# Optimization experiments

Hardware: AMD Instinct MI355X
Metric: run time of the kernel (lower is better)

The kernel has to match this reference:

```python
import jax, jax.numpy as jnp
import numpy as np

DIM = 1024

def setup_inputs() -> dict:
    key = jax.random.key(0)
    ks = jax.random.split(key, 7)
    s = 1.0 / np.sqrt(DIM)
    x = jax.random.normal(ks[0], (8, 2048, DIM), dtype=jnp.float32)
    Wq = jax.random.uniform(ks[1], (DIM, DIM), jnp.float32, -s, s)
    bq = jax.random.uniform(ks[2], (DIM,), jnp.float32, -s, s)
    Wk = jax.random.uniform(ks[3], (DIM, DIM), jnp.float32, -s, s)
    bk = jax.random.uniform(ks[4], (DIM,), jnp.float32, -s, s)
    Wv = jax.random.uniform(ks[5], (DIM, DIM), jnp.float32, -s, s)
    bv = jax.random.uniform(ks[6], (DIM,), jnp.float32, -s, s)
    return {"x": x, "Wq": Wq, "bq": bq, "Wk": Wk, "bk": bk, "Wv": Wv, "bv": bv}

def reference(x, Wq, bq, Wk, bk, Wv, bv):
    # nn.Linear: y = x @ W.T + b
    q = jnp.einsum('bsd,ed->bse', x, Wq) + bq  # [B,S,D]
    k = jnp.einsum('bsd,ed->bse', x, Wk) + bk
    v = jnp.einsum('bsd,ed->bse', x, Wv) + bv
    scores = jnp.einsum('bqd,bkd->bqk', q, k) / jnp.sqrt(jnp.float32(DIM))
    attn = jax.nn.softmax(scores, axis=-1)
    return jnp.einsum('bqk,bkd->bqd', attn, v)
```

## Files before the change

### kernel.cpp

```cpp
#include <hip/hip_runtime.h>

#define DIM 1024
#define SEQ 2048

typedef __attribute__((ext_vector_type(8))) short bf16x8;
typedef __attribute__((ext_vector_type(4))) float f32x4;
typedef __attribute__((ext_vector_type(4))) unsigned short us4;
typedef __attribute__((ext_vector_type(4))) _Float16 h4;

__device__ __forceinline__ unsigned short f2bf(float f) {
    union { float f; unsigned int u; } v; v.f = f;
    unsigned int r = (v.u + 0x7FFFu + ((v.u >> 16) & 1u)) >> 16;
    return (unsigned short)r;
}

#define GLOAD(gp, lp) __builtin_amdgcn_global_load_lds( \
    (const __attribute__((address_space(1))) unsigned int*)(gp), \
    (__attribute__((address_space(3))) unsigned int*)(lp), 16, 0, 0)

__global__ __launch_bounds__(256) void cast_f32_bf16(const float* __restrict__ src,
                                                     unsigned short* __restrict__ dst, int n) {
    int i = (blockIdx.x * 256 + threadIdx.x) * 8;
    if (i >= n) return;
    float4 a = *(const float4*)(src + i);
    float4 b = *(const float4*)(src + i + 4);
    us4 lo = { f2bf(a.x), f2bf(a.y), f2bf(a.z), f2bf(a.w) };
    us4 hi = { f2bf(b.x), f2bf(b.y), f2bf(b.z), f2bf(b.w) };
    *(us4*)(dst + i) = lo;
    *(us4*)(dst + i + 4) = hi;
}

#define STAGE4(sb, kt) do { \
    GLOAD(A + (size_t)(lr) * lda + (kt) + csrc,       smem + (sb) * 32768 + wid * 1024); \
    GLOAD(A + (size_t)(128 + lr) * lda + (kt) + csrc, smem + (sb) * 32768 + 8192 + wid * 1024); \
    GLOAD(B + (size_t)(lr) * ldb + (kt) + csrc,       smem + (sb) * 32768 + 16384 + wid * 1024); \
    GLOAD(B + (size_t)(128 + lr) * ldb + (kt) + csrc, smem + (sb) * 32768 + 24576 + wid * 1024); \
} while (0)

__device__ __forceinline__ void gemm256_core(
    const unsigned short* __restrict__ A, const unsigned short* __restrict__ B,
    int lda, int ldb, int K, char* smem, f32x4 acc[8][4])
{
    const int tid = threadIdx.x;
    const int lane = tid & 63;
    const int wid = tid >> 6;
    const int wm = wid >> 2;
    const int wn = wid & 3;
    const int lr = tid >> 2;
    const int csrc = ((tid & 3) ^ ((tid >> 3) & 3)) * 8;

    int aoff[8], boff[4];
    {
        int arow = wm * 128 + (lane & 15);
        int cr = (lane >> 4) ^ ((arow >> 1) & 3);
#pragma unroll
        for (int mi = 0; mi < 8; mi++) aoff[mi] = (arow + mi * 16) * 64 + cr * 16;
        int brow = wn * 64 + (lane & 15);
        int crb = (lane >> 4) ^ ((brow >> 1) & 3);
#pragma unroll
        for (int nj = 0; nj < 4; nj++) boff[nj] = 16384 + (brow + nj * 16) * 64 + crb * 16;
    }

    const int nph = K >> 5;

#pragma unroll
    for (int jb = 0; jb < 3; jb++) STAGE4(jb, jb * 32);

    for (int j = 0; j < nph; ++j) {
        if (j + 2 < nph)      asm volatile("s_waitcnt vmcnt(8)" ::: "memory");
        else if (j + 1 < nph) asm volatile("s_waitcnt vmcnt(4)" ::: "memory");
        else                  asm volatile("s_waitcnt vmcnt(0)" ::: "memory");
        __builtin_amdgcn_s_barrier();

        const char* bufb = smem + (j & 3) * 32768;
        bf16x8 af[8], bfr[4];
#pragma unroll
        for (int mi = 0; mi < 8; mi++) af[mi] = *(const bf16x8*)(bufb + aoff[mi]);
#pragma unroll
        for (int nj = 0; nj < 4; nj++) bfr[nj] = *(const bf16x8*)(bufb + boff[nj]);

        if (j + 3 < nph) STAGE4((j + 3) & 3, (j + 3) * 32);

        __builtin_amdgcn_s_setprio(1);
#pragma unroll
        for (int mi = 0; mi < 8; mi++)
#pragma unroll
            for (int nj = 0; nj < 4; nj++)
                acc[mi][nj] = __builtin_amdgcn_mfma_f32_16x16x32_bf16(af[mi], bfr[nj], acc[mi][nj], 0, 0, 0);
        __builtin_amdgcn_s_setprio(0);
    }
}

#define ACC_INIT() \
    f32x4 acc[8][4]; \
    _Pragma("unroll") for (int i = 0; i < 8; i++) \
    _Pragma("unroll") for (int jj = 0; jj < 4; jj++) acc[i][jj] = (f32x4){0.f, 0.f, 0.f, 0.f};

__global__ __launch_bounds__(512, 2) void gemm_qkv(
    const unsigned short* __restrict__ xb, const unsigned short* __restrict__ wb,
    const float* __restrict__ bq, const float* __restrict__ bk, const float* __restrict__ bv,
    unsigned short* __restrict__ qb, unsigned short* __restrict__ kb, unsigned short* __restrict__ vt)
{
    extern __shared__ char smem[];
    const int bid = blockIdx.x;
    const int lb = (bid & 7) * 96 + (bid >> 3);
    const int bz = lb >> 8;
    const int r = lb & 255;
    const int m0 = (r >> 2) * 256, n0 = (r & 3) * 256;
    const float* bias = (bz == 0) ? bq : ((bz == 1) ? bk : bv);
    ACC_INIT();
    gemm256_core(xb + (size_t)m0 * DIM, wb + (size_t)bz * DIM * DIM + (size_t)n0 * DIM,
                 DIM, DIM, DIM, smem, acc);
    const int lane = threadIdx.x & 63, wid = threadIdx.x >> 6;
    const int wm = wid >> 2, wn = wid & 3;
    const float scale = (bz == 0) ? 0.03125f : 1.0f;
    unsigned short* C = (bz == 0) ? qb : kb;
#pragma unroll
    for (int mig = 0; mig < 8; mig++)
#pragma unroll
        for (int nj = 0; nj < 4; nj++) {
            int col = n0 + wn * 64 + nj * 16 + (lane & 15);
            float bcol = bias[col];
#pragma unroll
            for (int rr = 0; rr < 4; rr++) {
                int row = m0 + wm * 128 + mig * 16 + (lane >> 4) * 4 + rr;
                float v = (acc[mig][nj][rr] + bcol) * scale;
                if (bz < 2) {
                    C[(size_t)row * DIM + col] = f2bf(v);
                } else {
                    int b = row >> 11, s = row & 2047;
                    vt[((size_t)b << 21) + ((size_t)col << 11) + s] = f2bf(v);
                }
            }
        }
}

__global__ __launch_bounds__(512, 2) void gemm_qk(
    const unsigned short* __restrict__ qb, const unsigned short* __restrict__ kb,
    unsigned short* __restrict__ sb)
{
    extern __shared__ char smem[];
    const int bid = blockIdx.x;
    const int lb = (bid & 7) * 64 + (bid >> 3);
    const int b = lb >> 6;
    const int r = lb & 63;
    const int m0 = (r >> 3) * 256, n0 = (r & 7) * 256;
    ACC_INIT();
    gemm256_core(qb + ((size_t)b * SEQ + m0) * DIM, kb + ((size_t)b * SEQ + n0) * DIM,
                 DIM, DIM, DIM, smem, acc);
    const int lane = threadIdx.x & 63, wid = threadIdx.x >> 6;
    const int wm = wid >> 2, wn = wid & 3;
    _Float16* sh = (_Float16*)sb + (size_t)b * SEQ * SEQ;
#pragma unroll
    for (int mig = 0; mig < 8; mig++)
#pragma unroll
        for (int nj = 0; nj < 4; nj++) {
            int col = n0 + wn * 64 + nj * 16 + (lane & 15);
#pragma unroll
            for (int rr = 0; rr < 4; rr++) {
                int row = m0 + wm * 128 + mig * 16 + (lane >> 4) * 4 + rr;
                sh[(size_t)row * SEQ + col] = (_Float16)acc[mig][nj][rr];
            }
        }
}

__global__ __launch_bounds__(256) void softmax_p(unsigned short* __restrict__ sb)
{
    const int lane = threadIdx.x & 63, wid = threadIdx.x >> 6;
    const size_t row = (size_t)blockIdx.x * 4 + wid;
    unsigned short* rp = sb + row * SEQ;
    float v[32];
#pragma unroll
    for (int j = 0; j < 8; j++) {
        h4 h = *(const h4*)(rp + (j * 64 + lane) * 4);
#pragma unroll
        for (int e = 0; e < 4; e++) v[j * 4 + e] = (float)h[e];
    }
    float m = -1e30f;
#pragma unroll
    for (int i = 0; i < 32; i++) m = fmaxf(m, v[i]);
#pragma unroll
    for (int msk = 1; msk <= 32; msk <<= 1) m = fmaxf(m, __shfl_xor(m, msk, 64));
    float s = 0.f;
#pragma unroll
    for (int i = 0; i < 32; i++) { v[i] = __expf(v[i] - m); s += v[i]; }
#pragma unroll
    for (int msk = 1; msk <= 32; msk <<= 1) s += __shfl_xor(s, msk, 64);
    float inv = 1.0f / s;
#pragma unroll
    for (int j = 0; j < 8; j++) {
        us4 pu = { f2bf(v[j * 4] * inv), f2bf(v[j * 4 + 1] * inv),
                   f2bf(v[j * 4 + 2] * inv), f2bf(v[j * 4 + 3] * inv) };
        *(us4*)(rp + (j * 64 + lane) * 4) = pu;
    }
}

__global__ __launch_bounds__(512, 2) void gemm_pv(
    const unsigned short* __restrict__ pb, const unsigned short* __restrict__ vt,
    float* __restrict__ out)
{
    extern __shared__ char smem[];
    const int bid = blockIdx.x;
    const int lb = (bid & 7) * 32 + (bid >> 3);
    const int b = lb >> 5;
    const int r = lb & 31;
    const int m0 = (r >> 2) * 256, n0 = (r & 3) * 256;
    ACC_INIT();
    gemm256_core(pb + ((size_t)b * SEQ + m0) * SEQ, vt + ((size_t)b * DIM + n0) * SEQ,
                 SEQ, SEQ, SEQ, smem, acc);
    const int lane = threadIdx.x & 63, wid = threadIdx.x >> 6;
    const int wm = wid >> 2, wn = wid & 3;
    float* O = out + (size_t)b * SEQ * DIM;
#pragma unroll
    for (int mig = 0; mig < 8; mig++)
#pragma unroll
        for (int nj = 0; nj < 4; nj++) {
            int col = n0 + wn * 64 + nj * 16 + (lane & 15);
#pragma unroll
            for (int rr = 0; rr < 4; rr++) {
                int row = m0 + wm * 128 + mig * 16 + (lane >> 4) * 4 + rr;
                O[(size_t)row * DIM + col] = acc[mig][nj][rr];
            }
        }
}

extern "C" void kernel_launch(void* const* d_in, const int* in_sizes, int n_in,
                              void* d_out, int out_size, void* d_ws, size_t ws_size,
                              hipStream_t stream) {
    const float* x  = (const float*)d_in[0];
    const float* Wq = (const float*)d_in[1];
    const float* bq = (const float*)d_in[2];
    const float* Wk = (const float*)d_in[3];
    const float* bk = (const float*)d_in[4];
    const float* Wv = (const float*)d_in[5];
    const float* bv = (const float*)d_in[6];
    float* out = (float*)d_out;
    char* ws = (char*)d_ws;

    unsigned short* xb = (unsigned short*)(ws);
    unsigned short* wb = (unsigned short*)(ws + 33554432);
    unsigned short* qb = (unsigned short*)(ws + 39845888);
    unsigned short* kb = (unsigned short*)(ws + 73400320);
    unsigned short* vt = (unsigned short*)(ws + 106954752);
    unsigned short* sb = (unsigned short*)(ws + 140509184);

    cast_f32_bf16<<<dim3(8192), 256, 0, stream>>>(x, xb, 16777216);
    cast_f32_bf16<<<dim3(512), 256, 0, stream>>>(Wq, wb, 1048576);
    cast_f32_bf16<<<dim3(512), 256, 0, stream>>>(Wk, wb + 1048576, 1048576);
    cast_f32_bf16<<<dim3(512), 256, 0, stream>>>(Wv, wb + 2097152, 1048576);

    hipFuncSetAttribute((const void*)gemm_qkv, hipFuncAttributeMaxDynamicSharedMemorySize, 131072);
    hipFuncSetAttribute((const void*)gemm_qk,  hipFuncAttributeMaxDynamicSharedMemorySize, 131072);
    hipFuncSetAttribute((const void*)gemm_pv,  hipFuncAttributeMaxDynamicSharedMemorySize, 131072);

    gemm_qkv<<<dim3(768), 512, 131072, stream>>>(xb, wb, bq, bk, bv, qb, kb, vt);
    gemm_qk<<<dim3(512), 512, 131072, stream>>>(qb, kb, sb);
    softmax_p<<<dim3(4096), 256, 0, stream>>>(sb);
    gemm_pv<<<dim3(256), 512, 131072, stream>>>(sb, vt, out);
}
```

Before: 350.6 us.

## Restructure GEMM core into 64-wide K tiles with quadrant-split ping-pong pipeline

The 256x256 GEMM main loop now uses K tiles of 64 instead of 32, with two 64KB LDS buffers instead of four 32KB stages. Each iteration is split into four MFMA quadrants, and half-tile global-to-LDS loads for the next A tile and the tile after next for B are issued between them, separated by barriers and scheduling fences. The XOR swizzle widens to 8 chunks to match 128-byte rows. The goal is to overlap loads with MFMA work at a finer grain and halve loop overhead. The cost is many more barriers per tile and a more fragile ordering of waitcnt and barriers, including A loaded one tile ahead and B two tiles ahead.

```diff
diff --git a/kernel.cpp b/kernel.cpp
--- a/kernel.cpp
+++ b/kernel.cpp
@@ -17,6 +17,8 @@
 #define GLOAD(gp, lp) __builtin_amdgcn_global_load_lds( \
     (const __attribute__((address_space(1))) unsigned int*)(gp), \
     (__attribute__((address_space(3))) unsigned int*)(lp), 16, 0, 0)
+
+#define MFMA(a, b, c) __builtin_amdgcn_mfma_f32_16x16x32_bf16((a), (b), (c), 0, 0, 0)
 
 __global__ __launch_bounds__(256) void cast_f32_bf16(const float* __restrict__ src,
                                                      unsigned short* __restrict__ dst, int n) {
@@ -30,11 +32,9 @@
     *(us4*)(dst + i + 4) = hi;
 }
 
-#define STAGE4(sb, kt) do { \
-    GLOAD(A + (size_t)(lr) * lda + (kt) + csrc,       smem + (sb) * 32768 + wid * 1024); \
-    GLOAD(A + (size_t)(128 + lr) * lda + (kt) + csrc, smem + (sb) * 32768 + 8192 + wid * 1024); \
-    GLOAD(B + (size_t)(lr) * ldb + (kt) + csrc,       smem + (sb) * 32768 + 16384 + wid * 1024); \
-    GLOAD(B + (size_t)(128 + lr) * ldb + (kt) + csrc, smem + (sb) * 32768 + 24576 + wid * 1024); \
+#define STAGE_HALF(G, ld, R0, kt, off) do { \
+    GLOAD((G) + (size_t)((R0) + (tid >> 3)) * (ld) + (kt) + csrc,      smem + (off) + tid * 16); \
+    GLOAD((G) + (size_t)((R0) + 64 + (tid >> 3)) * (ld) + (kt) + csrc, smem + (off) + 8192 + tid * 16); \
 } while (0)
 
 __device__ __forceinline__ void gemm256_core(
@@ -43,51 +43,112 @@
 {
     const int tid = threadIdx.x;
     const int lane = tid & 63;
-    const int wid = tid >> 6;
-    const int wm = wid >> 2;
-    const int wn = wid & 3;
-    const int lr = tid >> 2;
-    const int csrc = ((tid & 3) ^ ((tid >> 3) & 3)) * 8;
-
-    int aoff[8], boff[4];
-    {
-        int arow = wm * 128 + (lane & 15);
-        int cr = (lane >> 4) ^ ((arow >> 1) & 3);
-#pragma unroll
-        for (int mi = 0; mi < 8; mi++) aoff[mi] = (arow + mi * 16) * 64 + cr * 16;
-        int brow = wn * 64 + (lane & 15);
-        int crb = (lane >> 4) ^ ((brow >> 1) & 3);
-#pragma unroll
-        for (int nj = 0; nj < 4; nj++) boff[nj] = 16384 + (brow + nj * 16) * 64 + crb * 16;
-    }
-
-    const int nph = K >> 5;
-
-#pragma unroll
-    for (int jb = 0; jb < 3; jb++) STAGE4(jb, jb * 32);
-
-    for (int j = 0; j < nph; ++j) {
-        if (j + 2 < nph)      asm volatile("s_waitcnt vmcnt(8)" ::: "memory");
-        else if (j + 1 < nph) asm volatile("s_waitcnt vmcnt(4)" ::: "memory");
-        else                  asm volatile("s_waitcnt vmcnt(0)" ::: "memory");
-        __builtin_amdgcn_s_barrier();
-
-        const char* bufb = smem + (j & 3) * 32768;
-        bf16x8 af[8], bfr[4];
-#pragma unroll
-        for (int mi = 0; mi < 8; mi++) af[mi] = *(const bf16x8*)(bufb + aoff[mi]);
-#pragma unroll
-        for (int nj = 0; nj < 4; nj++) bfr[nj] = *(const bf16x8*)(bufb + boff[nj]);
-
-        if (j + 3 < nph) STAGE4((j + 3) & 3, (j + 3) * 32);
-
+    const int wm = (tid >> 6) >> 2;
+    const int wn = (tid >> 6) & 3;
+    const int csrc = ((tid & 7) ^ ((tid >> 3) & 7)) * 8;
+    const int NT = K >> 6;
+
+    const int arow = (wm * 128 + (lane & 15)) * 128;
+    const int brow = 32768 + (wn * 64 + (lane & 15)) * 128;
+    const int csw0 = (((lane >> 4) ^ (lane & 7)) * 16);
+    const int csw1 = (((4 + (lane >> 4)) ^ (lane & 7)) * 16);
+
+    bf16x8 af[8], b01[4], b23[4];
+
+    STAGE_HALF(A, lda, 0,   0, 0);
+    STAGE_HALF(A, lda, 128, 0, 16384);
+    STAGE_HALF(B, ldb, 0,   0, 32768);
+    STAGE_HALF(B, ldb, 128, 0, 49152);
+    STAGE_HALF(B, ldb, 0,   64, 65536 + 32768);
+    STAGE_HALF(B, ldb, 128, 64, 65536 + 49152);
+    asm volatile("s_waitcnt vmcnt(4)" ::: "memory");
+    __builtin_amdgcn_s_barrier();
+
+    for (int T = 0; T < NT; ++T) {
+        const char* db = smem + (T & 1) * 65536;
+        const int d1 = ((T + 1) & 1) * 65536;
+        const int d2 = (T & 1) * 65536;
+
+#pragma unroll
+        for (int mi = 0; mi < 4; mi++) {
+            af[mi * 2]     = *(const bf16x8*)(db + arow + mi * 2048 + csw0);
+            af[mi * 2 + 1] = *(const bf16x8*)(db + arow + mi * 2048 + csw1);
+        }
+#pragma unroll
+        for (int nj = 0; nj < 2; nj++) {
+            b01[nj * 2]     = *(const bf16x8*)(db + brow + nj * 2048 + csw0);
+            b01[nj * 2 + 1] = *(const bf16x8*)(db + brow + nj * 2048 + csw1);
+        }
+        if (T + 1 < NT) STAGE_HALF(A, lda, 0, (T + 1) * 64, d1);
+        asm volatile("s_waitcnt lgkmcnt(8)" ::: "memory");
+        __builtin_amdgcn_s_barrier();
+        asm volatile("s_waitcnt lgkmcnt(0)" ::: "memory");
+        __builtin_amdgcn_sched_barrier(0);
         __builtin_amdgcn_s_setprio(1);
 #pragma unroll
-        for (int mi = 0; mi < 8; mi++)
-#pragma unroll
-            for (int nj = 0; nj < 4; nj++)
-                acc[mi][nj] = __builtin_amdgcn_mfma_f32_16x16x32_bf16(af[mi], bfr[nj], acc[mi][nj], 0, 0, 0);
+        for (int ks = 0; ks < 2; ks++)
+#pragma unroll
+            for (int mi = 0; mi < 4; mi++)
+#pragma unroll
+                for (int nj = 0; nj < 2; nj++)
+                    acc[mi][nj] = MFMA(af[mi * 2 + ks], b01[nj * 2 + ks], acc[mi][nj]);
         __builtin_amdgcn_s_setprio(0);
+        __builtin_amdgcn_s_barrier();
+
+#pragma unroll
+        for (int nj = 0; nj < 2; nj++) {
+            b23[nj * 2]     = *(const bf16x8*)(db + brow + (nj + 2) * 2048 + csw0);
+            b23[nj * 2 + 1] = *(const bf16x8*)(db + brow + (nj + 2) * 2048 + csw1);
+        }
+        if (T + 1 < NT) STAGE_HALF(A, lda, 128, (T + 1) * 64, d1 + 16384);
+        __builtin_amdgcn_s_barrier();
+        asm volatile("s_waitcnt lgkmcnt(0)" ::: "memory");
+        __builtin_amdgcn_sched_barrier(0);
+        __builtin_amdgcn_s_setprio(1);
+#pragma unroll
+        for (int ks = 0; ks < 2; ks++)
+#pragma unroll
+            for (int mi = 0; mi < 4; mi++)
+#pragma unroll
+                for (int nj = 0; nj < 2; nj++)
+                    acc[mi][nj + 2] = MFMA(af[mi * 2 + ks], b23[nj * 2 + ks], acc[mi][nj + 2]);
+        __builtin_amdgcn_s_setprio(0);
+        __builtin_amdgcn_s_barrier();
+
+#pragma unroll
+        for (int mi = 0; mi < 4; mi++) {
+            af[mi * 2]     = *(const bf16x8*)(db + arow + (mi + 4) * 2048 + csw0);
+            af[mi * 2 + 1] = *(const bf16x8*)(db + arow + (mi + 4) * 2048 + csw1);
+        }
+        if (T + 2 < NT) STAGE_HALF(B, ldb, 0, (T + 2) * 64, d2 + 32768);
+        __builtin_amdgcn_s_barrier();
+        asm volatile("s_waitcnt lgkmcnt(0)" ::: "memory");
+        __builtin_amdgcn_sched_barrier(0);
+        __builtin_amdgcn_s_setprio(1);
+#pragma unroll
+        for (int ks = 0; ks < 2; ks++)
+#pragma unroll
+            for (int mi = 0; mi < 4; mi++)
+#pragma unroll
+                for (int nj = 0; nj < 2; nj++)
+                    acc[mi + 4][nj] = MFMA(af[mi * 2 + ks], b01[nj * 2 + ks], acc[mi + 4][nj]);
+        __builtin_amdgcn_s_setprio(0);
+        __builtin_amdgcn_s_barrier();
+
+        if (T + 2 < NT) STAGE_HALF(B, ldb, 128, (T + 2) * 64, d2 + 49152);
+        __builtin_amdgcn_s_barrier();
+        __builtin_amdgcn_s_setprio(1);
+#pragma unroll
+        for (int ks = 0; ks < 2; ks++)
+#pragma unroll
+            for (int mi = 0; mi < 4; mi++)
+#pragma unroll
+                for (int nj = 0; nj < 2; nj++)
+                    acc[mi + 4][nj + 2] = MFMA(af[mi * 2 + ks], b23[nj * 2 + ks], acc[mi + 4][nj + 2]);
+        __builtin_amdgcn_s_setprio(0);
+        if (T + 2 < NT) asm volatile("s_waitcnt vmcnt(4)" ::: "memory");
+        else            asm volatile("s_waitcnt vmcnt(0)" ::: "memory");
+        __builtin_amdgcn_s_barrier();
     }
 }
 
```

Measured after the change: 343.9 us. About the same (-1.9%).

## Switch GEMM core to 32x32x16 MFMA with shallower prefetch and split QKV launches

Applied to the files above, without the earlier changes.

The shared GEMM core now uses 32x32x16 bf16 MFMA tiles (4x2 per wave) in place of 16x16x32 tiles (8x4), changing the LDS fragment layout and swizzle and cutting LDS reads per MFMA. Prefetch depth drops from three stages in flight to two, with the next tile's loads issued before the fragment reads. The fused QKV kernel becomes three templated launches with the projection selected at compile time, removing runtime branching in the epilogue. The risks are less latency hiding from the shallower pipeline and three smaller grids (256 blocks each) in place of one larger one.

```diff
diff --git a/kernel.cpp b/kernel.cpp
--- a/kernel.cpp
+++ b/kernel.cpp
@@ -4,7 +4,7 @@
 #define SEQ 2048
 
 typedef __attribute__((ext_vector_type(8))) short bf16x8;
-typedef __attribute__((ext_vector_type(4))) float f32x4;
+typedef __attribute__((ext_vector_type(16))) float f32x16;
 typedef __attribute__((ext_vector_type(4))) unsigned short us4;
 typedef __attribute__((ext_vector_type(4))) _Float16 h4;
 
@@ -17,6 +17,8 @@
 #define GLOAD(gp, lp) __builtin_amdgcn_global_load_lds( \
     (const __attribute__((address_space(1))) unsigned int*)(gp), \
     (__attribute__((address_space(3))) unsigned int*)(lp), 16, 0, 0)
+
+#define MFMA32(a, b, c) __builtin_amdgcn_mfma_f32_32x32x16_bf16((a), (b), (c), 0, 0, 0)
 
 __global__ __launch_bounds__(256) void cast_f32_bf16(const float* __restrict__ src,
                                                      unsigned short* __restrict__ dst, int n) {
@@ -30,106 +32,114 @@
     *(us4*)(dst + i + 4) = hi;
 }
 
-#define STAGE4(sb, kt) do { \
-    GLOAD(A + (size_t)(lr) * lda + (kt) + csrc,       smem + (sb) * 32768 + wid * 1024); \
-    GLOAD(A + (size_t)(128 + lr) * lda + (kt) + csrc, smem + (sb) * 32768 + 8192 + wid * 1024); \
-    GLOAD(B + (size_t)(lr) * ldb + (kt) + csrc,       smem + (sb) * 32768 + 16384 + wid * 1024); \
-    GLOAD(B + (size_t)(128 + lr) * ldb + (kt) + csrc, smem + (sb) * 32768 + 24576 + wid * 1024); \
-} while (0)
-
 __device__ __forceinline__ void gemm256_core(
     const unsigned short* __restrict__ A, const unsigned short* __restrict__ B,
-    int lda, int ldb, int K, char* smem, f32x4 acc[8][4])
+    int lda, int ldb, int K, char* smem, f32x16 acc[4][2])
 {
     const int tid = threadIdx.x;
     const int lane = tid & 63;
-    const int wid = tid >> 6;
-    const int wm = wid >> 2;
-    const int wn = wid & 3;
-    const int lr = tid >> 2;
-    const int csrc = ((tid & 3) ^ ((tid >> 3) & 3)) * 8;
-
-    int aoff[8], boff[4];
-    {
-        int arow = wm * 128 + (lane & 15);
-        int cr = (lane >> 4) ^ ((arow >> 1) & 3);
-#pragma unroll
-        for (int mi = 0; mi < 8; mi++) aoff[mi] = (arow + mi * 16) * 64 + cr * 16;
-        int brow = wn * 64 + (lane & 15);
-        int crb = (lane >> 4) ^ ((brow >> 1) & 3);
-#pragma unroll
-        for (int nj = 0; nj < 4; nj++) boff[nj] = 16384 + (brow + nj * 16) * 64 + crb * 16;
-    }
-
-    const int nph = K >> 5;
-
-#pragma unroll
-    for (int jb = 0; jb < 3; jb++) STAGE4(jb, jb * 32);
-
-    for (int j = 0; j < nph; ++j) {
-        if (j + 2 < nph)      asm volatile("s_waitcnt vmcnt(8)" ::: "memory");
-        else if (j + 1 < nph) asm volatile("s_waitcnt vmcnt(4)" ::: "memory");
-        else                  asm volatile("s_waitcnt vmcnt(0)" ::: "memory");
+    const int wm = (tid >> 6) >> 2;
+    const int wn = (tid >> 6) & 3;
+    const int l31 = lane & 31, lhi = lane >> 5;
+
+    const int srow = tid >> 2;
+    const int schunk = ((tid & 3) ^ (srow & 3)) * 8;
+    const unsigned short* pa0 = A + (size_t)srow * lda + schunk;
+    const unsigned short* pa1 = A + (size_t)(128 + srow) * lda + schunk;
+    const unsigned short* pb0 = B + (size_t)srow * ldb + schunk;
+    const unsigned short* pb1 = B + (size_t)(128 + srow) * ldb + schunk;
+    const int doff = tid * 16;
+
+    const int abase = (wm * 128 + l31) * 64;
+    const int bbase = 16384 + (wn * 64 + l31) * 64;
+    const int csw0 = (lhi ^ (l31 & 3)) * 16;
+    const int csw1 = ((2 + lhi) ^ (l31 & 3)) * 16;
+
+    const int NT = K >> 5;
+
+#define STAGE32(bufi, kt) do { \
+    char* d = smem + (bufi) * 32768 + doff; \
+    GLOAD(pa0 + (kt), d); \
+    GLOAD(pa1 + (kt), d + 8192); \
+    GLOAD(pb0 + (kt), d + 16384); \
+    GLOAD(pb1 + (kt), d + 24576); \
+} while (0)
+
+    STAGE32(0, 0);
+    STAGE32(1, 32);
+
+    for (int T = 0; T < NT; ++T) {
+        if (T + 1 < NT) asm volatile("s_waitcnt vmcnt(4)" ::: "memory");
+        else            asm volatile("s_waitcnt vmcnt(0)" ::: "memory");
         __builtin_amdgcn_s_barrier();
 
-        const char* bufb = smem + (j & 3) * 32768;
-        bf16x8 af[8], bfr[4];
-#pragma unroll
-        for (int mi = 0; mi < 8; mi++) af[mi] = *(const bf16x8*)(bufb + aoff[mi]);
-#pragma unroll
-        for (int nj = 0; nj < 4; nj++) bfr[nj] = *(const bf16x8*)(bufb + boff[nj]);
-
-        if (j + 3 < nph) STAGE4((j + 3) & 3, (j + 3) * 32);
+        if (T + 2 < NT) STAGE32((T + 2) & 3, (T + 2) * 32);
+
+        const char* db = smem + (T & 3) * 32768;
+        bf16x8 a0[4], a1[4], b0[2], b1[2];
+#pragma unroll
+        for (int mi = 0; mi < 4; mi++) {
+            a0[mi] = *(const bf16x8*)(db + abase + mi * 2048 + csw0);
+            a1[mi] = *(const bf16x8*)(db + abase + mi * 2048 + csw1);
+        }
+#pragma unroll
+        for (int nj = 0; nj < 2; nj++) {
+            b0[nj] = *(const bf16x8*)(db + bbase + nj * 2048 + csw0);
+            b1[nj] = *(const bf16x8*)(db + bbase + nj * 2048 + csw1);
+        }
 
         __builtin_amdgcn_s_setprio(1);
 #pragma unroll
-        for (int mi = 0; mi < 8; mi++)
-#pragma unroll
-            for (int nj = 0; nj < 4; nj++)
-                acc[mi][nj] = __builtin_amdgcn_mfma_f32_16x16x32_bf16(af[mi], bfr[nj], acc[mi][nj], 0, 0, 0);
+        for (int mi = 0; mi < 4; mi++)
+#pragma unroll
+            for (int nj = 0; nj < 2; nj++)
+                acc[mi][nj] = MFMA32(a0[mi], b0[nj], acc[mi][nj]);
+#pragma unroll
+        for (int mi = 0; mi < 4; mi++)
+#pragma unroll
+            for (int nj = 0; nj < 2; nj++)
+                acc[mi][nj] = MFMA32(a1[mi], b1[nj], acc[mi][nj]);
         __builtin_amdgcn_s_setprio(0);
     }
+#undef STAGE32
 }
 
 #define ACC_INIT() \
-    f32x4 acc[8][4]; \
-    _Pragma("unroll") for (int i = 0; i < 8; i++) \
-    _Pragma("unroll") for (int jj = 0; jj < 4; jj++) acc[i][jj] = (f32x4){0.f, 0.f, 0.f, 0.f};
-
-__global__ __launch_bounds__(512, 2) void gemm_qkv(
-    const unsigned short* __restrict__ xb, const unsigned short* __restrict__ wb,
-    const float* __restrict__ bq, const float* __restrict__ bk, const float* __restrict__ bv,
-    unsigned short* __restrict__ qb, unsigned short* __restrict__ kb, unsigned short* __restrict__ vt)
+    f32x16 acc[4][2]; \
+    _Pragma("unroll") for (int i = 0; i < 4; i++) \
+    _Pragma("unroll") for (int jj = 0; jj < 2; jj++) acc[i][jj] = (f32x16){}; \
+
+
+template<int BZ>
+__global__ __launch_bounds__(512, 2) void gemm_qkv_t(
+    const unsigned short* __restrict__ xb, const unsigned short* __restrict__ w,
+    const float* __restrict__ bias, unsigned short* __restrict__ C)
 {
     extern __shared__ char smem[];
     const int bid = blockIdx.x;
-    const int lb = (bid & 7) * 96 + (bid >> 3);
-    const int bz = lb >> 8;
-    const int r = lb & 255;
-    const int m0 = (r >> 2) * 256, n0 = (r & 3) * 256;
-    const float* bias = (bz == 0) ? bq : ((bz == 1) ? bk : bv);
+    const int lb = (bid & 7) * 32 + (bid >> 3);
+    const int m0 = (lb >> 2) * 256, n0 = (lb & 3) * 256;
     ACC_INIT();
-    gemm256_core(xb + (size_t)m0 * DIM, wb + (size_t)bz * DIM * DIM + (size_t)n0 * DIM,
-                 DIM, DIM, DIM, smem, acc);
+    gemm256_core(xb + (size_t)m0 * DIM, w + (size_t)n0 * DIM, DIM, DIM, DIM, smem, acc);
     const int lane = threadIdx.x & 63, wid = threadIdx.x >> 6;
     const int wm = wid >> 2, wn = wid & 3;
-    const float scale = (bz == 0) ? 0.03125f : 1.0f;
-    unsigned short* C = (bz == 0) ? qb : kb;
-#pragma unroll
-    for (int mig = 0; mig < 8; mig++)
-#pragma unroll
-        for (int nj = 0; nj < 4; nj++) {
-            int col = n0 + wn * 64 + nj * 16 + (lane & 15);
-            float bcol = bias[col];
-#pragma unroll
-            for (int rr = 0; rr < 4; rr++) {
-                int row = m0 + wm * 128 + mig * 16 + (lane >> 4) * 4 + rr;
-                float v = (acc[mig][nj][rr] + bcol) * scale;
-                if (bz < 2) {
+    const int l31 = lane & 31, lhi = lane >> 5;
+    const float scale = (BZ == 0) ? 0.03125f : 1.0f;
+#pragma unroll
+    for (int mi = 0; mi < 4; mi++)
+#pragma unroll
+        for (int nj = 0; nj < 2; nj++) {
+            const int col = n0 + wn * 64 + nj * 32 + l31;
+            const float bcol = bias[col];
+#pragma unroll
+            for (int r = 0; r < 16; r++) {
+                const int row = m0 + wm * 128 + mi * 32 + (r & 3) + 8 * (r >> 2) + 4 * lhi;
+                const float v = (acc[mi][nj][r] + bcol) * scale;
+                if (BZ < 2) {
                     C[(size_t)row * DIM + col] = f2bf(v);
                 } else {
-                    int b = row >> 11, s = row & 2047;
-                    vt[((size_t)b << 21) + ((size_t)col << 11) + s] = f2bf(v);
+                    const int b = row >> 11, s = row & 2047;
+                    C[((size_t)b << 21) + ((size_t)col << 11) + s] = f2bf(v);
                 }
             }
         }
@@ -143,23 +153,24 @@
     const int bid = blockIdx.x;
     const int lb = (bid & 7) * 64 + (bid >> 3);
     const int b = lb >> 6;
-    const int r = lb & 63;
-    const int m0 = (r >> 3) * 256, n0 = (r & 7) * 256;
+    const int r0 = lb & 63;
+    const int m0 = (r0 >> 3) * 256, n0 = (r0 & 7) * 256;
     ACC_INIT();
     gemm256_core(qb + ((size_t)b * SEQ + m0) * DIM, kb + ((size_t)b * SEQ + n0) * DIM,
                  DIM, DIM, DIM, smem, acc);
     const int lane = threadIdx.x & 63, wid = threadIdx.x >> 6;
     const int wm = wid >> 2, wn = wid & 3;
+    const int l31 = lane & 31, lhi = lane >> 5;
     _Float16* sh = (_Float16*)sb + (size_t)b * SEQ * SEQ;
 #pragma unroll
-    for (int mig = 0; mig < 8; mig++)
-#pragma unroll
-        for (int nj = 0; nj < 4; nj++) {
-            int col = n0 + wn * 64 + nj * 16 + (lane & 15);
-#pragma unroll
-            for (int rr = 0; rr < 4; rr++) {
-                int row = m0 + wm * 128 + mig * 16 + (lane >> 4) * 4 + rr;
-                sh[(size_t)row * SEQ + col] = (_Float16)acc[mig][nj][rr];
+    for (int mi = 0; mi < 4; mi++)
+#pragma unroll
+        for (int nj = 0; nj < 2; nj++) {
+            const int col = n0 + wn * 64 + nj * 32 + l31;
+#pragma unroll
+            for (int r = 0; r < 16; r++) {
+                const int row = m0 + wm * 128 + mi * 32 + (r & 3) + 8 * (r >> 2) + 4 * lhi;
+                sh[(size_t)row * SEQ + col] = (_Float16)acc[mi][nj][r];
             }
         }
 }
@@ -203,23 +214,24 @@
     const int bid = blockIdx.x;
     const int lb = (bid & 7) * 32 + (bid >> 3);
     const int b = lb >> 5;
-    const int r = lb & 31;
-    const int m0 = (r >> 2) * 256, n0 = (r & 3) * 256;
+    const int r0 = lb & 31;
+    const int m0 = (r0 >> 2) * 256, n0 = (r0 & 3) * 256;
     ACC_INIT();
     gemm256_core(pb + ((size_t)b * SEQ + m0) * SEQ, vt + ((size_t)b * DIM + n0) * SEQ,
                  SEQ, SEQ, SEQ, smem, acc);
     const int lane = threadIdx.x & 63, wid = threadIdx.x >> 6;
     const int wm = wid >> 2, wn = wid & 3;
+    const int l31 = lane & 31, lhi = lane >> 5;
     float* O = out + (size_t)b * SEQ * DIM;
 #pragma unroll
-    for (int mig = 0; mig < 8; mig++)
-#pragma unroll
-        for (int nj = 0; nj < 4; nj++) {
-            int col = n0 + wn * 64 + nj * 16 + (lane & 15);
-#pragma unroll
-            for (int rr = 0; rr < 4; rr++) {
-                int row = m0 + wm * 128 + mig * 16 + (lane >> 4) * 4 + rr;
-                O[(size_t)row * DIM + col] = acc[mig][nj][rr];
+    for (int mi = 0; mi < 4; mi++)
+#pragma unroll
+        for (int nj = 0; nj < 2; nj++) {
+            const int col = n0 + wn * 64 + nj * 32 + l31;
+#pragma unroll
+            for (int r = 0; r < 16; r++) {
+                const int row = m0 + wm * 128 + mi * 32 + (r & 3) + 8 * (r >> 2) + 4 * lhi;
+                O[(size_t)row * DIM + col] = acc[mi][nj][r];
             }
         }
 }
@@ -249,11 +261,15 @@
     cast_f32_bf16<<<dim3(512), 256, 0, stream>>>(Wk, wb + 1048576, 1048576);
     cast_f32_bf16<<<dim3(512), 256, 0, stream>>>(Wv, wb + 2097152, 1048576);
 
-    hipFuncSetAttribute((const void*)gemm_qkv, hipFuncAttributeMaxDynamicSharedMemorySize, 131072);
+    hipFuncSetAttribute((const void*)gemm_qkv_t<0>, hipFuncAttributeMaxDynamicSharedMemorySize, 131072);
+    hipFuncSetAttribute((const void*)gemm_qkv_t<1>, hipFuncAttributeMaxDynamicSharedMemorySize, 131072);
+    hipFuncSetAttribute((const void*)gemm_qkv_t<2>, hipFuncAttributeMaxDynamicSharedMemorySize, 131072);
     hipFuncSetAttribute((const void*)gemm_qk,  hipFuncAttributeMaxDynamicSharedMemorySize, 131072);
     hipFuncSetAttribute((const void*)gemm_pv,  hipFuncAttributeMaxDynamicSharedMemorySize, 131072);
 
-    gemm_qkv<<<dim3(768), 512, 131072, stream>>>(xb, wb, bq, bk, bv, qb, kb, vt);
+    gemm_qkv_t<0><<<dim3(256), 512, 131072, stream>>>(xb, wb,           bq, qb);
+    gemm_qkv_t<1><<<dim3(256), 512, 131072, stream>>>(xb, wb + 1048576, bk, kb);
+    gemm_qkv_t<2><<<dim3(256), 512, 131072, stream>>>(xb, wb + 2097152, bv, vt);
     gemm_qk<<<dim3(512), 512, 131072, stream>>>(qb, kb, sb);
     softmax_p<<<dim3(4096), 256, 0, stream>>>(sb);
     gemm_pv<<<dim3(256), 512, 131072, stream>>>(sb, vt, out);
```

Result: faster. 336.9 us (-3.9%).
